# Kernel tuning notes

Measured on AMD Instinct MI355X. Metric: run time of the kernel, lower is better.

The kernel has to match this reference:

```python
import jax, jax.numpy as jnp
import numpy as np

B, IH, IW = 16, 32, 32
N = IH * IW
HEADS, DIM_HEAD = 8, 64
INNER = HEADS * DIM_HEAD  # 512
INP, OUP = 512, 512
SCALE = DIM_HEAD ** -0.5


def _relative_index():
    # replicate torch.meshgrid (ij) -> coords [2, N]
    yy, xx = np.meshgrid(np.arange(IH), np.arange(IW), indexing='ij')
    coords = np.stack([yy.reshape(-1), xx.reshape(-1)])  # [2, N]
    rel = coords[:, :, None] - coords[:, None, :]        # [2, N, N]
    rel[0] += IH - 1
    rel[1] += IW - 1
    rel[0] *= 2 * IW - 1
    return jnp.asarray(rel.sum(0).reshape(-1), dtype=jnp.int32)  # [N*N]


def setup_inputs() -> dict:
    key = jax.random.key(0)
    k1, k2, k3, k4, k5 = jax.random.split(key, 5)
    x = jax.random.normal(k1, (B, N, INP), dtype=jnp.float32)
    W_qkv = jax.random.normal(k2, (INP, 3 * INNER), dtype=jnp.float32) * (INP ** -0.5)
    # table is initialized to zeros in the module; use small randn so bias path is exercised
    rel_table = jax.random.normal(k3, ((2 * IH - 1) * (2 * IW - 1), HEADS), dtype=jnp.float32) * 0.02
    W_out = jax.random.normal(k4, (INNER, OUP), dtype=jnp.float32) * (INNER ** -0.5)
    b_out = jax.random.normal(k5, (OUP,), dtype=jnp.float32) * 0.02
    return {
        'x': x,
        'W_qkv': W_qkv,
        'rel_table': rel_table,
        'W_out': W_out,
        'b_out': b_out,
        'rel_index': _relative_index(),
    }


def reference(x, W_qkv, rel_table, W_out, b_out, rel_index):
    b, n, _ = x.shape
    qkv = x @ W_qkv                                            # [b, n, 3*inner]
    q, k, v = jnp.split(qkv, 3, axis=-1)
    def to_heads(t):
        return t.reshape(b, n, HEADS, DIM_HEAD).transpose(0, 2, 1, 3)  # [b, h, n, d]
    q, k, v = to_heads(q), to_heads(k), to_heads(v)
    dots = jnp.einsum('bhnd,bhmd->bhnm', q, k) * SCALE         # [b, h, n, n]
    bias = rel_table[rel_index].reshape(n, n, HEADS).transpose(2, 0, 1)[None]  # [1, h, n, n]
    attn = jax.nn.softmax(dots + bias, axis=-1)
    out = jnp.einsum('bhnm,bhmd->bhnd', attn, v)               # [b, h, n, d]
    out = out.transpose(0, 2, 1, 3).reshape(b, n, INNER)       # [b, n, inner]
    return out @ W_out + b_out
```

## Files before the change

kernel.cpp:

```cpp
#include <hip/hip_runtime.h>
#include <math.h>

#define BATCH 16
#define NTOK 1024
#define HEADS 8
#define DHEAD 64
#define INNER 512
#define QKV_COLS 1536
#define SCALE_L2E 0.1803368801111244f
#define LOG2E 1.4426950408889634f

#if __has_builtin(__builtin_amdgcn_exp2f)
#define EXP2F(x) __builtin_amdgcn_exp2f(x)
#else
#define EXP2F(x) __expf((x) * 0.6931471805599453f)
#endif

typedef _Float16 f16x8 __attribute__((ext_vector_type(8)));
typedef _Float16 f16x4 __attribute__((ext_vector_type(4)));
typedef float f32x4 __attribute__((ext_vector_type(4)));

#define MFMA32(a, b, c) __builtin_amdgcn_mfma_f32_16x16x32_f16(a, b, c, 0, 0, 0)

__device__ __forceinline__ void glds16(const void* g, void* l) {
    __builtin_amdgcn_global_load_lds(
        (const __attribute__((address_space(1))) unsigned int*)g,
        (__attribute__((address_space(3))) unsigned int*)l, 16, 0, 0);
}

#define XV (BATCH * NTOK * INNER / 4)
#define WQ (INNER * QKV_COLS)
#define WO (INNER * INNER)

__global__ __launch_bounds__(256)
void convert_inputs(const float* __restrict__ x, const float* __restrict__ Wq,
                    const float* __restrict__ Wo, _Float16* __restrict__ x_h,
                    _Float16* __restrict__ Wq_t, _Float16* __restrict__ Wo_t) {
    int idx = blockIdx.x * 256 + threadIdx.x;
    if (idx < XV) {
        float4 v = ((const float4*)x)[idx];
        f16x4 h;
        h[0] = (_Float16)v.x; h[1] = (_Float16)v.y;
        h[2] = (_Float16)v.z; h[3] = (_Float16)v.w;
        *(f16x4*)(x_h + (size_t)idx * 4) = h;
    } else if (idx < XV + WQ) {
        int i = idx - XV;
        int n = i >> 9, k = i & 511;
        Wq_t[i] = (_Float16)Wq[k * QKV_COLS + n];
    } else if (idx < XV + WQ + WO) {
        int i = idx - XV - WQ;
        int n = i >> 9, k = i & 511;
        Wo_t[i] = (_Float16)Wo[k * INNER + n];
    }
}

template<int MODE>
__global__ __launch_bounds__(256, 4)
void gemm_f16(const _Float16* __restrict__ A, const _Float16* __restrict__ Bt,
              const float* __restrict__ bias, void* __restrict__ Cout,
              _Float16* __restrict__ vtg, int M, int N, int K) {
    __shared__ _Float16 As[2][128 * 32];
    __shared__ _Float16 Bs[2][128 * 32];

    const int t    = threadIdx.x;
    const int l    = t & 63;
    const int w    = t >> 6;
    const int wm   = w >> 1;
    const int wn   = w & 1;
    const int quad = l >> 4;
    const int lrow = l & 15;

    const int nwg = gridDim.x * gridDim.y;
    int bid = blockIdx.x + gridDim.x * blockIdx.y;
    bid = (bid & 7) * (nwg >> 3) + (bid >> 3);
    const size_t row0 = (size_t)(bid / gridDim.x) * 128;
    const size_t col0 = (size_t)(bid % gridDim.x) * 128;

    const int srow = t >> 2;
    const int sch  = t & 3;

    f32x4 acc[4][4] = {};

    const int NSTEP = K >> 5;

    auto stage = [&](int kk, int bufi) {
        const int k0 = kk * 32;
#pragma unroll
        for (int p = 0; p < 2; ++p) {
            const int r  = p * 64 + srow;
            const int gc = (sch ^ (r & 3)) * 8;
            glds16(A  + (row0 + r) * K + k0 + gc, (char*)As[bufi] + p * 4096 + t * 16);
            glds16(Bt + (col0 + r) * K + k0 + gc, (char*)Bs[bufi] + p * 4096 + t * 16);
        }
    };

    stage(0, 0);

    for (int kk = 0; kk < NSTEP; ++kk) {
        const int buf = kk & 1;
        __syncthreads();
        if (kk + 1 < NSTEP) stage(kk + 1, buf ^ 1);

        f16x8 af[4], bf[4];
#pragma unroll
        for (int i = 0; i < 4; ++i) {
            const int r = wm * 64 + i * 16 + lrow;
            af[i] = *(const f16x8*)(As[buf] + r * 32 + ((quad ^ (r & 3)) * 8));
        }
#pragma unroll
        for (int j = 0; j < 4; ++j) {
            const int r = wn * 64 + j * 16 + lrow;
            bf[j] = *(const f16x8*)(Bs[buf] + r * 32 + ((quad ^ (r & 3)) * 8));
        }
#pragma unroll
        for (int i = 0; i < 4; ++i)
#pragma unroll
            for (int j = 0; j < 4; ++j)
                acc[i][j] = MFMA32(bf[j], af[i], acc[i][j]);
    }

    const bool isV = (MODE == 2) && (col0 >= 2 * INNER);
#pragma unroll
    for (int i = 0; i < 4; ++i) {
        const size_t m = row0 + wm * 64 + i * 16 + lrow;
#pragma unroll
        for (int j = 0; j < 4; ++j) {
            const size_t c = col0 + wn * 64 + j * 16 + quad * 4;
            f32x4 v = acc[i][j];
            if (MODE == 0) {
                float4 bv = *(const float4*)(bias + c);
                v[0] += bv.x; v[1] += bv.y; v[2] += bv.z; v[3] += bv.w;
                *(f32x4*)((float*)Cout + m * N + c) = v;
            } else if (!isV) {
                f16x4 hv;
                hv[0] = (_Float16)v[0]; hv[1] = (_Float16)v[1];
                hv[2] = (_Float16)v[2]; hv[3] = (_Float16)v[3];
                *(f16x4*)((_Float16*)Cout + m * N + c) = hv;
            } else {
                const int cv = (int)(c - 2 * INNER);
                const int hh = cv >> 6, db = cv & 63;
                const size_t vb = (((size_t)(m >> 10) * HEADS + hh) * 64 + db) * NTOK
                                  + (m & (NTOK - 1));
#pragma unroll
                for (int reg = 0; reg < 4; ++reg)
                    vtg[vb + (size_t)reg * NTOK] = (_Float16)v[reg];
            }
        }
    }
}

__global__ __launch_bounds__(512, 4)
void attn_f16_v6(const _Float16* __restrict__ qkv, const _Float16* __restrict__ vt,
                 const float* __restrict__ rel_table, _Float16* __restrict__ out) {
    __shared__ _Float16 Ks[2][64 * 64];
    __shared__ _Float16 Vs[2][64 * 64];
    __shared__ float biasS[3969];

    const int t    = threadIdx.x;
    const int l    = t & 63;
    const int w    = t >> 6;
    const int quad = l >> 4;
    const int lrow = l & 15;
    const int h    = blockIdx.y;
    const int bb   = blockIdx.z;
    const int qr0  = blockIdx.x * 256 + w * 32;

    for (int idx = t; idx < 3969; idx += 512)
        biasS[idx] = rel_table[idx * HEADS + h] * LOG2E;

    const size_t tokbase = (size_t)bb * NTOK;

    f16x8 aq[2][2];
#pragma unroll
    for (int mt = 0; mt < 2; ++mt)
#pragma unroll
        for (int ksi = 0; ksi < 2; ++ksi)
            aq[mt][ksi] = *(const f16x8*)(qkv + (tokbase + qr0 + mt * 16 + lrow) * QKV_COLS
                                          + h * DHEAD + ksi * 32 + quad * 8);

    f32x4 O[2][4] = {};
    float l0 = 0.f, l1 = 0.f;

    const int iy = qr0 >> 5;
    const int krow_base = 8 * (lrow >> 2) + (lrow & 3);
    const int fKl = (lrow & 3) + 4 * ((lrow >> 2) & 1);

    const int kr  = t >> 3;
    const int ksl = t & 7;
    const int fKr = (kr & 3) + 4 * ((kr >> 3) & 1);
    const _Float16* kbase = qkv + tokbase * QKV_COLS + INNER + h * DHEAD;
    const _Float16* vbase = vt + ((size_t)(bb * HEADS + h) * 64) * NTOK;

    auto stage = [&](int jt, int bufi) {
        const int j0s = jt * 64;
        glds16(kbase + (size_t)(j0s + kr) * QKV_COLS + (ksl ^ fKr) * 8, (char*)Ks[bufi] + t * 16);
        glds16(vbase + (size_t)kr * NTOK + j0s + (ksl ^ (kr & 7)) * 8,  (char*)Vs[bufi] + t * 16);
    };

    stage(0, 0);

    for (int jt = 0; jt < 16; ++jt) {
        const int buf = jt & 1;
        __syncthreads();
        if (jt < 15) stage(jt + 1, buf ^ 1);

#pragma unroll
        for (int jn0 = 0; jn0 < 2; ++jn0) {
            f16x8 pb0, pb1;
#pragma unroll
            for (int s = 0; s < 2; ++s) {
                const int krow = jn0 * 32 + krow_base + 4 * s;
                f32x4 S0 = {}, S1 = {};
#pragma unroll
                for (int ksi = 0; ksi < 2; ++ksi) {
                    f16x8 bk = *(const f16x8*)(Ks[buf] + krow * 64
                                               + (((ksi * 4 + quad) ^ fKl) * 8));
                    S0 = MFMA32(bk, aq[0][ksi], S0);
                    S1 = MFMA32(bk, aq[1][ksi], S1);
                }
                const int base = (iy - (jt * 2 + jn0) + 31) * 63 + 31 + lrow
                                 - 8 * quad - 4 * s;
                {
                    float p0 = EXP2F(fmaf(S0[0], SCALE_L2E, biasS[base - 0]));
                    float p1 = EXP2F(fmaf(S0[1], SCALE_L2E, biasS[base - 1]));
                    float p2 = EXP2F(fmaf(S0[2], SCALE_L2E, biasS[base - 2]));
                    float p3 = EXP2F(fmaf(S0[3], SCALE_L2E, biasS[base - 3]));
                    l0 += (p0 + p1) + (p2 + p3);
                    pb0[s * 4 + 0] = (_Float16)p0; pb0[s * 4 + 1] = (_Float16)p1;
                    pb0[s * 4 + 2] = (_Float16)p2; pb0[s * 4 + 3] = (_Float16)p3;
                }
                {
                    const int b1 = base + 16;
                    float p0 = EXP2F(fmaf(S1[0], SCALE_L2E, biasS[b1 - 0]));
                    float p1 = EXP2F(fmaf(S1[1], SCALE_L2E, biasS[b1 - 1]));
                    float p2 = EXP2F(fmaf(S1[2], SCALE_L2E, biasS[b1 - 2]));
                    float p3 = EXP2F(fmaf(S1[3], SCALE_L2E, biasS[b1 - 3]));
                    l1 += (p0 + p1) + (p2 + p3);
                    pb1[s * 4 + 0] = (_Float16)p0; pb1[s * 4 + 1] = (_Float16)p1;
                    pb1[s * 4 + 2] = (_Float16)p2; pb1[s * 4 + 3] = (_Float16)p3;
                }
            }

#pragma unroll
            for (int dn = 0; dn < 4; ++dn) {
                const int d = dn * 16 + lrow;
                f16x8 av = *(const f16x8*)(Vs[buf] + d * 64
                              + (((jn0 * 4 + quad) ^ (d & 7)) * 8));
                O[0][dn] = MFMA32(av, pb0, O[0][dn]);
                O[1][dn] = MFMA32(av, pb1, O[1][dn]);
            }
        }
    }

#pragma unroll
    for (int mt = 0; mt < 2; ++mt) {
        float s = mt ? l1 : l0;
        s += __shfl_xor(s, 16);
        s += __shfl_xor(s, 32);
        const float inv = 1.f / s;
        const size_t orow = (tokbase + qr0 + mt * 16 + lrow) * INNER + h * DHEAD;
#pragma unroll
        for (int dn = 0; dn < 4; ++dn) {
            const f32x4 o = O[mt][dn];
            f16x4 ov;
            ov[0] = (_Float16)(o[0] * inv); ov[1] = (_Float16)(o[1] * inv);
            ov[2] = (_Float16)(o[2] * inv); ov[3] = (_Float16)(o[3] * inv);
            *(f16x4*)(out + orow + dn * 16 + quad * 4) = ov;
        }
    }
}

extern "C" void kernel_launch(void* const* d_in, const int* in_sizes, int n_in,
                              void* d_out, int out_size, void* d_ws, size_t ws_size,
                              hipStream_t stream) {
    const float* x         = (const float*)d_in[0];
    const float* W_qkv     = (const float*)d_in[1];
    const float* rel_table = (const float*)d_in[2];
    const float* W_out     = (const float*)d_in[3];
    const float* b_out     = (const float*)d_in[4];

    _Float16* x_h   = (_Float16*)d_ws;
    _Float16* Wq_t  = x_h + (size_t)BATCH * NTOK * INNER;
    _Float16* Wo_t  = Wq_t + (size_t)INNER * QKV_COLS;
    _Float16* qkv_h = Wo_t + (size_t)INNER * INNER;
    _Float16* att_h = qkv_h + (size_t)BATCH * NTOK * QKV_COLS;
    _Float16* vt_g  = att_h + (size_t)BATCH * NTOK * INNER;

    const int M = BATCH * NTOK;

    convert_inputs<<<(XV + WQ + WO + 255) / 256, 256, 0, stream>>>(
        x, W_qkv, W_out, x_h, Wq_t, Wo_t);

    gemm_f16<2><<<dim3(QKV_COLS / 128, M / 128), 256, 0, stream>>>(
        x_h, Wq_t, nullptr, qkv_h, vt_g, M, QKV_COLS, INNER);

    attn_f16_v6<<<dim3(NTOK / 256, HEADS, BATCH), 512, 0, stream>>>(
        qkv_h, vt_g, rel_table, att_h);

    gemm_f16<0><<<dim3(INNER / 128, M / 128), 256, 0, stream>>>(
        att_h, Wo_t, b_out, d_out, nullptr, M, INNER, INNER);
}
```

Measured before the change: 206.8 us.

## Fuse fp32-to-fp16 conversion of x into QKV GEMM and add MFMA priority hints

The separate pass that converted x to fp16 is removed. The QKV GEMM now loads fp32 rows of x into registers, converts them, and writes the fp16 result into shared memory after the MFMA block, so the next tile's load overlaps compute. This drops one write and one read of the 16 MB fp16 copy of x, but the GEMM now reads twice the bytes for A and uses register-staged loads instead of direct-to-LDS loads. The attention kernel also brackets its MFMA sections with s_setprio so those waves get higher scheduling priority.

```diff
diff --git a/kernel.cpp b/kernel.cpp
--- a/kernel.cpp
+++ b/kernel.cpp
@@ -28,27 +28,18 @@
         (__attribute__((address_space(3))) unsigned int*)l, 16, 0, 0);
 }
 
-#define XV (BATCH * NTOK * INNER / 4)
 #define WQ (INNER * QKV_COLS)
 #define WO (INNER * INNER)
 
 __global__ __launch_bounds__(256)
-void convert_inputs(const float* __restrict__ x, const float* __restrict__ Wq,
-                    const float* __restrict__ Wo, _Float16* __restrict__ x_h,
-                    _Float16* __restrict__ Wq_t, _Float16* __restrict__ Wo_t) {
+void convert_w(const float* __restrict__ Wq, const float* __restrict__ Wo,
+               _Float16* __restrict__ Wq_t, _Float16* __restrict__ Wo_t) {
     int idx = blockIdx.x * 256 + threadIdx.x;
-    if (idx < XV) {
-        float4 v = ((const float4*)x)[idx];
-        f16x4 h;
-        h[0] = (_Float16)v.x; h[1] = (_Float16)v.y;
-        h[2] = (_Float16)v.z; h[3] = (_Float16)v.w;
-        *(f16x4*)(x_h + (size_t)idx * 4) = h;
-    } else if (idx < XV + WQ) {
-        int i = idx - XV;
-        int n = i >> 9, k = i & 511;
-        Wq_t[i] = (_Float16)Wq[k * QKV_COLS + n];
-    } else if (idx < XV + WQ + WO) {
-        int i = idx - XV - WQ;
+    if (idx < WQ) {
+        int n = idx >> 9, k = idx & 511;
+        Wq_t[idx] = (_Float16)Wq[k * QKV_COLS + n];
+    } else if (idx < WQ + WO) {
+        int i = idx - WQ;
         int n = i >> 9, k = i & 511;
         Wo_t[i] = (_Float16)Wo[k * INNER + n];
     }
@@ -56,9 +47,10 @@
 
 template<int MODE>
 __global__ __launch_bounds__(256, 4)
-void gemm_f16(const _Float16* __restrict__ A, const _Float16* __restrict__ Bt,
-              const float* __restrict__ bias, void* __restrict__ Cout,
-              _Float16* __restrict__ vtg, int M, int N, int K) {
+void gemm_f16(const _Float16* __restrict__ A, const float* __restrict__ Af,
+              const _Float16* __restrict__ Bt, const float* __restrict__ bias,
+              void* __restrict__ Cout, _Float16* __restrict__ vtg,
+              int M, int N, int K) {
     __shared__ _Float16 As[2][128 * 32];
     __shared__ _Float16 Bs[2][128 * 32];
 
@@ -80,26 +72,59 @@
     const int sch  = t & 3;
 
     f32x4 acc[4][4] = {};
-
     const int NSTEP = K >> 5;
 
-    auto stage = [&](int kk, int bufi) {
-        const int k0 = kk * 32;
+    float4 ar[2][2];
+
+    auto loadA = [&](int kk, int bufi) {
+        if (MODE == 2) {
+#pragma unroll
+            for (int p = 0; p < 2; ++p) {
+                const float* s = Af + (row0 + p * 64 + srow) * K + kk * 32 + sch * 8;
+                ar[p][0] = *(const float4*)s;
+                ar[p][1] = *(const float4*)(s + 4);
+            }
+        } else {
+#pragma unroll
+            for (int p = 0; p < 2; ++p) {
+                const int r  = p * 64 + srow;
+                const int gc = (sch ^ (r & 3)) * 8;
+                glds16(A + (row0 + r) * K + kk * 32 + gc,
+                       (char*)As[bufi] + p * 4096 + t * 16);
+            }
+        }
+    };
+    auto writeA = [&](int bufi) {
+#pragma unroll
+        for (int p = 0; p < 2; ++p) {
+            const int r = p * 64 + srow;
+            f16x8 h;
+#pragma unroll
+            for (int e = 0; e < 4; ++e) {
+                h[e]     = (_Float16)ar[p][0][e];
+                h[4 + e] = (_Float16)ar[p][1][e];
+            }
+            *(f16x8*)(As[bufi] + r * 32 + ((sch ^ (r & 3)) * 8)) = h;
+        }
+    };
+    auto stageB = [&](int kk, int bufi) {
 #pragma unroll
         for (int p = 0; p < 2; ++p) {
             const int r  = p * 64 + srow;
             const int gc = (sch ^ (r & 3)) * 8;
-            glds16(A  + (row0 + r) * K + k0 + gc, (char*)As[bufi] + p * 4096 + t * 16);
-            glds16(Bt + (col0 + r) * K + k0 + gc, (char*)Bs[bufi] + p * 4096 + t * 16);
+            glds16(Bt + (col0 + r) * K + kk * 32 + gc,
+                   (char*)Bs[bufi] + p * 4096 + t * 16);
         }
     };
 
-    stage(0, 0);
+    loadA(0, 0);
+    stageB(0, 0);
+    if (MODE == 2) writeA(0);
 
     for (int kk = 0; kk < NSTEP; ++kk) {
         const int buf = kk & 1;
         __syncthreads();
-        if (kk + 1 < NSTEP) stage(kk + 1, buf ^ 1);
+        if (kk + 1 < NSTEP) { stageB(kk + 1, buf ^ 1); loadA(kk + 1, buf ^ 1); }
 
         f16x8 af[4], bf[4];
 #pragma unroll
@@ -117,6 +142,8 @@
 #pragma unroll
             for (int j = 0; j < 4; ++j)
                 acc[i][j] = MFMA32(bf[j], af[i], acc[i][j]);
+
+        if (MODE == 2 && kk + 1 < NSTEP) writeA(buf ^ 1);
     }
 
     const bool isV = (MODE == 2) && (col0 >= 2 * INNER);
@@ -150,7 +177,7 @@
 }
 
 __global__ __launch_bounds__(512, 4)
-void attn_f16_v6(const _Float16* __restrict__ qkv, const _Float16* __restrict__ vt,
+void attn_f16_v7(const _Float16* __restrict__ qkv, const _Float16* __restrict__ vt,
                  const float* __restrict__ rel_table, _Float16* __restrict__ out) {
     __shared__ _Float16 Ks[2][64 * 64];
     __shared__ _Float16 Vs[2][64 * 64];
@@ -211,6 +238,7 @@
             for (int s = 0; s < 2; ++s) {
                 const int krow = jn0 * 32 + krow_base + 4 * s;
                 f32x4 S0 = {}, S1 = {};
+                __builtin_amdgcn_s_setprio(1);
 #pragma unroll
                 for (int ksi = 0; ksi < 2; ++ksi) {
                     f16x8 bk = *(const f16x8*)(Ks[buf] + krow * 64
@@ -218,6 +246,7 @@
                     S0 = MFMA32(bk, aq[0][ksi], S0);
                     S1 = MFMA32(bk, aq[1][ksi], S1);
                 }
+                __builtin_amdgcn_s_setprio(0);
                 const int base = (iy - (jt * 2 + jn0) + 31) * 63 + 31 + lrow
                                  - 8 * quad - 4 * s;
                 {
@@ -241,6 +270,7 @@
                 }
             }
 
+            __builtin_amdgcn_s_setprio(1);
 #pragma unroll
             for (int dn = 0; dn < 4; ++dn) {
                 const int d = dn * 16 + lrow;
@@ -249,6 +279,7 @@
                 O[0][dn] = MFMA32(av, pb0, O[0][dn]);
                 O[1][dn] = MFMA32(av, pb1, O[1][dn]);
             }
+            __builtin_amdgcn_s_setprio(0);
         }
     }
 
@@ -279,8 +310,7 @@
     const float* W_out     = (const float*)d_in[3];
     const float* b_out     = (const float*)d_in[4];
 
-    _Float16* x_h   = (_Float16*)d_ws;
-    _Float16* Wq_t  = x_h + (size_t)BATCH * NTOK * INNER;
+    _Float16* Wq_t  = (_Float16*)d_ws;
     _Float16* Wo_t  = Wq_t + (size_t)INNER * QKV_COLS;
     _Float16* qkv_h = Wo_t + (size_t)INNER * INNER;
     _Float16* att_h = qkv_h + (size_t)BATCH * NTOK * QKV_COLS;
@@ -288,15 +318,14 @@
 
     const int M = BATCH * NTOK;
 
-    convert_inputs<<<(XV + WQ + WO + 255) / 256, 256, 0, stream>>>(
-        x, W_qkv, W_out, x_h, Wq_t, Wo_t);
+    convert_w<<<(WQ + WO + 255) / 256, 256, 0, stream>>>(W_qkv, W_out, Wq_t, Wo_t);
 
     gemm_f16<2><<<dim3(QKV_COLS / 128, M / 128), 256, 0, stream>>>(
-        x_h, Wq_t, nullptr, qkv_h, vt_g, M, QKV_COLS, INNER);
-
-    attn_f16_v6<<<dim3(NTOK / 256, HEADS, BATCH), 512, 0, stream>>>(
+        nullptr, x, Wq_t, nullptr, qkv_h, vt_g, M, QKV_COLS, INNER);
+
+    attn_f16_v7<<<dim3(NTOK / 256, HEADS, BATCH), 512, 0, stream>>>(
         qkv_h, vt_g, rel_table, att_h);
 
     gemm_f16<0><<<dim3(INNER / 128, M / 128), 256, 0, stream>>>(
-        att_h, Wo_t, b_out, d_out, nullptr, M, INNER, INNER);
-}
+        att_h, nullptr, Wo_t, b_out, d_out, nullptr, M, INNER, INNER);
+}
```

Measured after the change: 213.4 us. +3.2%, slower.

## Triple-buffer GEMM loads with vmcnt waits and prioritize attention MFMAs

Applied to the files above, without the earlier changes.

The GEMM moves from a double-buffered LDS pipeline with __syncthreads to three stages with explicit s_waitcnt vmcnt and raw barriers, prefetching two k-steps ahead. The LDS swizzle changes to use (r>>1)&3, and the occupancy hint drops from 4 to 3 blocks. The attention kernel wraps its MFMA sections in s_setprio so waves issuing matrix ops get scheduling priority. The aim is to hide global-load latency and keep the matrix units busy, at the cost of more LDS and lower occupancy. The single raw barrier per step may not fully protect the buffer being overwritten.

```diff
diff --git a/kernel.cpp b/kernel.cpp
--- a/kernel.cpp
+++ b/kernel.cpp
@@ -55,12 +55,12 @@
 }
 
 template<int MODE>
-__global__ __launch_bounds__(256, 4)
+__global__ __launch_bounds__(256, 3)
 void gemm_f16(const _Float16* __restrict__ A, const _Float16* __restrict__ Bt,
               const float* __restrict__ bias, void* __restrict__ Cout,
               _Float16* __restrict__ vtg, int M, int N, int K) {
-    __shared__ _Float16 As[2][128 * 32];
-    __shared__ _Float16 Bs[2][128 * 32];
+    __shared__ _Float16 As[3][128 * 32];
+    __shared__ _Float16 Bs[3][128 * 32];
 
     const int t    = threadIdx.x;
     const int l    = t & 63;
@@ -80,43 +80,48 @@
     const int sch  = t & 3;
 
     f32x4 acc[4][4] = {};
-
     const int NSTEP = K >> 5;
 
     auto stage = [&](int kk, int bufi) {
-        const int k0 = kk * 32;
 #pragma unroll
         for (int p = 0; p < 2; ++p) {
             const int r  = p * 64 + srow;
-            const int gc = (sch ^ (r & 3)) * 8;
-            glds16(A  + (row0 + r) * K + k0 + gc, (char*)As[bufi] + p * 4096 + t * 16);
-            glds16(Bt + (col0 + r) * K + k0 + gc, (char*)Bs[bufi] + p * 4096 + t * 16);
+            const int gc = (sch ^ ((r >> 1) & 3)) * 8;
+            glds16(A  + (row0 + r) * K + kk * 32 + gc, (char*)As[bufi] + p * 4096 + t * 16);
+            glds16(Bt + (col0 + r) * K + kk * 32 + gc, (char*)Bs[bufi] + p * 4096 + t * 16);
         }
     };
 
     stage(0, 0);
-
+    stage(1, 1);
+
+    int buf = 0, pre = 2;
     for (int kk = 0; kk < NSTEP; ++kk) {
-        const int buf = kk & 1;
-        __syncthreads();
-        if (kk + 1 < NSTEP) stage(kk + 1, buf ^ 1);
+        if (kk + 1 < NSTEP) asm volatile("s_waitcnt vmcnt(4)" ::: "memory");
+        else                asm volatile("s_waitcnt vmcnt(0)" ::: "memory");
+        __builtin_amdgcn_s_barrier();
+        __builtin_amdgcn_sched_barrier(0);
+        if (kk + 2 < NSTEP) stage(kk + 2, pre);
 
         f16x8 af[4], bf[4];
 #pragma unroll
         for (int i = 0; i < 4; ++i) {
             const int r = wm * 64 + i * 16 + lrow;
-            af[i] = *(const f16x8*)(As[buf] + r * 32 + ((quad ^ (r & 3)) * 8));
+            af[i] = *(const f16x8*)(As[buf] + r * 32 + ((quad ^ ((r >> 1) & 3)) * 8));
         }
 #pragma unroll
         for (int j = 0; j < 4; ++j) {
             const int r = wn * 64 + j * 16 + lrow;
-            bf[j] = *(const f16x8*)(Bs[buf] + r * 32 + ((quad ^ (r & 3)) * 8));
+            bf[j] = *(const f16x8*)(Bs[buf] + r * 32 + ((quad ^ ((r >> 1) & 3)) * 8));
         }
 #pragma unroll
         for (int i = 0; i < 4; ++i)
 #pragma unroll
             for (int j = 0; j < 4; ++j)
                 acc[i][j] = MFMA32(bf[j], af[i], acc[i][j]);
+
+        buf = (buf == 2) ? 0 : buf + 1;
+        pre = (pre == 2) ? 0 : pre + 1;
     }
 
     const bool isV = (MODE == 2) && (col0 >= 2 * INNER);
@@ -150,7 +155,7 @@
 }
 
 __global__ __launch_bounds__(512, 4)
-void attn_f16_v6(const _Float16* __restrict__ qkv, const _Float16* __restrict__ vt,
+void attn_f16_v7(const _Float16* __restrict__ qkv, const _Float16* __restrict__ vt,
                  const float* __restrict__ rel_table, _Float16* __restrict__ out) {
     __shared__ _Float16 Ks[2][64 * 64];
     __shared__ _Float16 Vs[2][64 * 64];
@@ -211,6 +216,7 @@
             for (int s = 0; s < 2; ++s) {
                 const int krow = jn0 * 32 + krow_base + 4 * s;
                 f32x4 S0 = {}, S1 = {};
+                __builtin_amdgcn_s_setprio(1);
 #pragma unroll
                 for (int ksi = 0; ksi < 2; ++ksi) {
                     f16x8 bk = *(const f16x8*)(Ks[buf] + krow * 64
@@ -218,6 +224,7 @@
                     S0 = MFMA32(bk, aq[0][ksi], S0);
                     S1 = MFMA32(bk, aq[1][ksi], S1);
                 }
+                __builtin_amdgcn_s_setprio(0);
                 const int base = (iy - (jt * 2 + jn0) + 31) * 63 + 31 + lrow
                                  - 8 * quad - 4 * s;
                 {
@@ -241,6 +248,7 @@
                 }
             }
 
+            __builtin_amdgcn_s_setprio(1);
 #pragma unroll
             for (int dn = 0; dn < 4; ++dn) {
                 const int d = dn * 16 + lrow;
@@ -249,6 +257,7 @@
                 O[0][dn] = MFMA32(av, pb0, O[0][dn]);
                 O[1][dn] = MFMA32(av, pb1, O[1][dn]);
             }
+            __builtin_amdgcn_s_setprio(0);
         }
     }
 
@@ -294,7 +303,7 @@
     gemm_f16<2><<<dim3(QKV_COLS / 128, M / 128), 256, 0, stream>>>(
         x_h, Wq_t, nullptr, qkv_h, vt_g, M, QKV_COLS, INNER);
 
-    attn_f16_v6<<<dim3(NTOK / 256, HEADS, BATCH), 512, 0, stream>>>(
+    attn_f16_v7<<<dim3(NTOK / 256, HEADS, BATCH), 512, 0, stream>>>(
         qkv_h, vt_g, rel_table, att_h);
 
     gemm_f16<0><<<dim3(INNER / 128, M / 128), 256, 0, stream>>>(
```

Result: no change. 205.6 us (-0.6%).
